# Performance work log

Measured on AMD Instinct MI355X. Metric: run time of the kernel, lower is better.

The kernel has to match this reference:

```python
import jax, jax.numpy as jnp
import numpy as np

B, S, D, H = 4, 2048, 512, 8


def _ln(x, g, b, eps=1e-5):
    m = x.mean(-1, keepdims=True)
    v = ((x - m) ** 2).mean(-1, keepdims=True)
    return (x - m) / jnp.sqrt(v + eps) * g + b


def setup_inputs() -> dict:
    key = jax.random.key(0)
    ks = iter(jax.random.split(key, 32))
    n = lambda shape, s=0.02: jax.random.normal(next(ks), shape, jnp.float32) * s
    z = lambda *shape: jnp.zeros(shape, jnp.float32)
    o = lambda *shape: jnp.ones(shape, jnp.float32)
    return {
        "x": jax.random.normal(next(ks), (B, S, D), jnp.float32),
        "x_prev": jax.random.normal(next(ks), (B, S, D), jnp.float32),
        "mu": jnp.float32(0.5),
        "in_proj_w": n((3 * D, D)), "in_proj_b": z(3 * D),
        "out_w": n((D, D)), "out_b": z(D),
        "ln1_g": o(D), "ln1_b": z(D),
        "time_mod": jnp.full((D,), 0.5, jnp.float32),
        "sm_ln_g": o(D), "sm_ln_b": z(D),
        "wr_w": n((D, D)), "wr_b": z(D),
        "wv_w": n((D, D)), "wv_b": z(D),
        "sc_ln_g": o(D), "sc_ln_b": z(D),
        "ln2_g": o(D), "ln2_b": z(D),
        "w1": n((4 * D, D)), "b1": z(4 * D),
        "w2": n((D, 4 * D)), "b2": z(D),
        "ln3_g": o(D), "ln3_b": z(D),
    }


def reference(x, x_prev, mu, in_proj_w, in_proj_b, out_w, out_b, ln1_g, ln1_b,
              time_mod, sm_ln_g, sm_ln_b, wr_w, wr_b, wv_w, wv_b,
              sc_ln_g, sc_ln_b, ln2_g, ln2_b, w1, b1, w2, b2, ln3_g, ln3_b):
    Bs, Sl, Dm = x.shape
    hd = Dm // H
    # Shift (x_prev is not None)
    shifted = mu * x + (1.0 - mu) * x_prev
    # Multihead self-attention (eval mode; dropout = identity)
    qkv = shifted @ in_proj_w.T + in_proj_b
    q, k, v = jnp.split(qkv, 3, axis=-1)
    q = q.reshape(Bs, Sl, H, hd)
    k = k.reshape(Bs, Sl, H, hd)
    v = v.reshape(Bs, Sl, H, hd)
    scores = jnp.einsum('bqhd,bkhd->bhqk', q, k) / jnp.sqrt(jnp.float32(hd))
    attn = jax.nn.softmax(scores, axis=-1)
    ao = jnp.einsum('bhqk,bkhd->bqhd', attn, v).reshape(Bs, Sl, Dm)
    ao = ao @ out_w.T + out_b
    x1 = _ln(shifted + ao, ln1_g, ln1_b)
    # SequenceMergingSeq with C = V = W = x1: sequential decayed running sums
    def step(carry, xt):  # xt: [B, D]
        a, b = carry
        decay = jax.nn.sigmoid(xt * time_mod)
        e = jnp.exp(xt)
        a = decay.mean(-1, keepdims=True) * a + e.sum(-1, keepdims=True)
        b = decay * b + e * xt
        return (a, b), b / (a + 1e-8)
    a0 = jnp.zeros((Bs, 1), x1.dtype)
    b0 = jnp.zeros((Bs, Dm), x1.dtype)
    _, outs = jax.lax.scan(step, (a0, b0), jnp.swapaxes(x1, 0, 1))  # [S,B,D]
    merged = _ln(jnp.swapaxes(outs, 0, 1), sm_ln_g, sm_ln_b)
    # StateCoupling
    coupled = _ln(jax.nn.sigmoid(merged @ wr_w.T + wr_b) * (merged @ wv_w.T + wv_b),
                  sc_ln_g, sc_ln_b)
    x2 = _ln(x1 + coupled, ln2_g, ln2_b)
    # FFN
    ffn = jax.nn.relu(x2 @ w1.T + b1) @ w2.T + b2
    return _ln(x2 + ffn, ln3_g, ln3_b)
```

## Files before the change

kernel.cpp:

```cpp
#include <hip/hip_runtime.h>
#include <math.h>

#define D_MODEL 512
#define SEQ     2048
#define BATCH   4
#define NH      8
#define HD      64
#define CHUNK   32
#define NCHUNK  64
#define M_TOK   (BATCH*SEQ)

typedef __attribute__((ext_vector_type(8))) short bhalf8;
typedef __attribute__((ext_vector_type(4))) float f32x4;

__device__ __forceinline__ float sigmoidf_(float x){ return 1.f/(1.f+expf(-x)); }

__device__ __forceinline__ unsigned short f2b(float f){
  unsigned u = __float_as_uint(f);
  u += 0x7FFFu + ((u>>16)&1u);
  return (unsigned short)(u>>16);
}
__device__ __forceinline__ float b2f(unsigned short h){
  return __uint_as_float(((unsigned)h)<<16);
}

__device__ __forceinline__ void gll16(const void* g, void* l){
  __builtin_amdgcn_global_load_lds(
      (const __attribute__((address_space(1))) unsigned int*)g,
      (__attribute__((address_space(3))) unsigned int*)l, 16, 0, 0);
}

__device__ __forceinline__ float exp2_hw(float x){
  float r;
  asm volatile("v_exp_f32 %0, %1" : "=v"(r) : "v"(x));
  return r;
}

__device__ __forceinline__ void block_sum2(float& a, float& b, float* lds){
  #pragma unroll
  for (int o=32;o>0;o>>=1){ a += __shfl_xor(a,o); b += __shfl_xor(b,o); }
  int w = threadIdx.x>>6, l = threadIdx.x&63;
  if (l==0){ lds[2*w]=a; lds[2*w+1]=b; }
  __syncthreads();
  float ta=0.f, tb=0.f; int nw = blockDim.x>>6;
  for (int i=0;i<nw;++i){ ta+=lds[2*i]; tb+=lds[2*i+1]; }
  a=ta; b=tb;
  __syncthreads();
}

__global__ void cvtshift_k(const float* __restrict__ s0,const float* __restrict__ s1,
                           const float* __restrict__ s2,const float* __restrict__ s3,
                           const float* __restrict__ s4,const float* __restrict__ s5,
                           unsigned short* __restrict__ d0,unsigned short* __restrict__ d1,
                           unsigned short* __restrict__ d2,unsigned short* __restrict__ d3,
                           unsigned short* __restrict__ d4,unsigned short* __restrict__ d5,
                           const float* __restrict__ x, const float* __restrict__ xp,
                           const float* __restrict__ mu, float* __restrict__ of,
                           unsigned short* __restrict__ ob){
  int t = blockIdx.x*blockDim.x + threadIdx.x;
  if (t < 917504){
    int j = t;
    const float* s; unsigned short* d;
    if (j < 196608){ s=s0; d=d0; }
    else if ((j-=196608) < 65536){ s=s1; d=d1; }
    else if ((j-=65536)  < 65536){ s=s2; d=d2; }
    else if ((j-=65536)  < 65536){ s=s3; d=d3; }
    else if ((j-=65536)  < 262144){ s=s4; d=d4; }
    else { j-=262144; s=s5; d=d5; }
    float4 v = ((const float4*)s)[j];
    unsigned a=f2b(v.x), b=f2b(v.y), c=f2b(v.z), e=f2b(v.w);
    uint2 p; p.x = a | (b<<16); p.y = c | (e<<16);
    ((uint2*)d)[j] = p;
  } else {
    int i = t - 917504;
    float m = mu[0];
    float4 a = ((const float4*)x)[i], p = ((const float4*)xp)[i];
    float4 r;
    r.x = m*a.x + (1.f-m)*p.x; r.y = m*a.y + (1.f-m)*p.y;
    r.z = m*a.z + (1.f-m)*p.z; r.w = m*a.w + (1.f-m)*p.w;
    ((float4*)of)[i] = r;
    unsigned A=f2b(r.x), B=f2b(r.y), C=f2b(r.z), E=f2b(r.w);
    uint2 q; q.x = A | (B<<16); q.y = C | (E<<16);
    ((uint2*)ob)[i] = q;
  }
}

template<int ACT, int OUTB>
__global__ __launch_bounds__(256) void mgemm_k(const unsigned short* __restrict__ A,
    const unsigned short* __restrict__ W, const float* __restrict__ bias,
    float* __restrict__ Yf, unsigned short* __restrict__ Yb, int Nd, int K){
  __shared__ unsigned short As[128*64];
  __shared__ unsigned short Bs[128*64];
  const int tid = threadIdx.x;
  const int w = tid>>6, lane = tid&63;
  const int l15 = lane&15, l4 = lane>>4;
  const int wr = w>>1, wc = w&1;
  const int nwg = gridDim.x*gridDim.y;
  const int orig = blockIdx.y*gridDim.x + blockIdx.x;
  const int swz = (orig&7)*(nwg>>3) + (orig>>3);
  const int bn = swz % gridDim.x;
  const int bm = swz / gridDim.x;

  const size_t Kb = (size_t)K*2;
  const int srow  = lane>>3;
  const int sbyte = ((lane&7)*16) ^ (srow<<4);
  const char* Ag = (const char*)A + (size_t)(bm*128)*Kb + sbyte;
  const char* Wg = (const char*)W + (size_t)(bn*128)*Kb + sbyte;

  f32x4 acc[4][4];
  const f32x4 z = {0.f,0.f,0.f,0.f};
  #pragma unroll
  for (int i=0;i<4;++i)
    #pragma unroll
    for (int j=0;j<4;++j) acc[i][j] = z;

  const int KT = K/64;
  for (int kt=0; kt<KT; ++kt){
    if (kt) __syncthreads();
    const size_t kOff = (size_t)kt*128;
    #pragma unroll
    for (int i=0;i<4;++i){
      int c = w*4 + i;
      int r = c*8 + srow;
      gll16(Ag + (size_t)r*Kb + kOff, (char*)As + c*1024);
      gll16(Wg + (size_t)r*Kb + kOff, (char*)Bs + c*1024);
    }
    __syncthreads();

    bhalf8 af[4][2], bf_[4][2];
    #pragma unroll
    for (int fr=0; fr<4; ++fr){
      int row = wr*64 + fr*16 + l15;
      #pragma unroll
      for (int ks=0; ks<2; ++ks){
        int byo = (l4*16 + ks*64) ^ ((row&7)<<4);
        af[fr][ks] = *(const bhalf8*)((const char*)As + row*128 + byo);
      }
    }
    #pragma unroll
    for (int fc=0; fc<4; ++fc){
      int row = wc*64 + fc*16 + l15;
      #pragma unroll
      for (int ks=0; ks<2; ++ks){
        int byo = (l4*16 + ks*64) ^ ((row&7)<<4);
        bf_[fc][ks] = *(const bhalf8*)((const char*)Bs + row*128 + byo);
      }
    }
    #pragma unroll
    for (int ks=0; ks<2; ++ks)
      #pragma unroll
      for (int fr=0; fr<4; ++fr)
        #pragma unroll
        for (int fc=0; fc<4; ++fc)
          acc[fr][fc] = __builtin_amdgcn_mfma_f32_16x16x32_bf16(af[fr][ks], bf_[fc][ks], acc[fr][fc], 0, 0, 0);
  }

  const int rowBase = bm*128 + wr*64;
  const int colBase = bn*128 + wc*64;
  #pragma unroll
  for (int fc=0; fc<4; ++fc){
    int col = colBase + fc*16 + l15;
    float bv = bias[col];
    #pragma unroll
    for (int fr=0; fr<4; ++fr){
      #pragma unroll
      for (int j=0; j<4; ++j){
        int row = rowBase + fr*16 + l4*4 + j;
        float v = acc[fr][fc][j] + bv;
        if (ACT) v = fmaxf(v, 0.f);
        if (OUTB) Yb[(size_t)row*Nd + col] = f2b(v);
        else      Yf[(size_t)row*Nd + col] = v;
      }
    }
  }
}

template<int ACT, int FUSE2, int OUTB>
__global__ __launch_bounds__(256) void mgemm64_k(const unsigned short* __restrict__ A,
    const unsigned short* __restrict__ W0, const unsigned short* __restrict__ W1v,
    const float* __restrict__ bias0, const float* __restrict__ bias1,
    float* __restrict__ Y0, float* __restrict__ Y1,
    unsigned short* __restrict__ Yb0, unsigned short* __restrict__ Yb1,
    int Nd, int K){
  __shared__ unsigned short As[128*64];
  __shared__ unsigned short Bs[64*64];
  const int tid = threadIdx.x;
  const int w = tid>>6, lane = tid&63;
  const int l15 = lane&15, l4 = lane>>4;
  const int wr = w>>1, wc = w&1;
  const int nwg = gridDim.x*gridDim.y;
  const int orig = blockIdx.y*gridDim.x + blockIdx.x;
  const int swz = (orig&7)*(nwg>>3) + (orig>>3);
  int bn = swz % gridDim.x;
  const int bm = swz / gridDim.x;
  const unsigned short* W = W0;
  const float* bias = bias0;
  float* Yf = Y0;
  unsigned short* Yb = Yb0;
  if (FUSE2 && bn >= 8){ W = W1v; bias = bias1; Yf = Y1; Yb = Yb1; bn -= 8; }

  const size_t Kb = (size_t)K*2;
  const int srow  = lane>>3;
  const int sbyte = ((lane&7)*16) ^ (srow<<4);
  const char* Ag = (const char*)A + (size_t)(bm*128)*Kb + sbyte;
  const char* Wg = (const char*)W + (size_t)(bn*64)*Kb + sbyte;

  f32x4 acc[4][2];
  const f32x4 z = {0.f,0.f,0.f,0.f};
  #pragma unroll
  for (int i=0;i<4;++i)
    #pragma unroll
    for (int j=0;j<2;++j) acc[i][j] = z;

  const int KT = K/64;
  for (int kt=0; kt<KT; ++kt){
    if (kt) __syncthreads();
    const size_t kOff = (size_t)kt*128;
    #pragma unroll
    for (int i=0;i<4;++i){
      int c = w*4 + i;
      int r = c*8 + srow;
      gll16(Ag + (size_t)r*Kb + kOff, (char*)As + c*1024);
    }
    #pragma unroll
    for (int i=0;i<2;++i){
      int c = w*2 + i;
      int r = c*8 + srow;
      gll16(Wg + (size_t)r*Kb + kOff, (char*)Bs + c*1024);
    }
    __syncthreads();

    bhalf8 af[4][2], bf_[2][2];
    #pragma unroll
    for (int fr=0; fr<4; ++fr){
      int row = wr*64 + fr*16 + l15;
      #pragma unroll
      for (int ks=0; ks<2; ++ks){
        int byo = (l4*16 + ks*64) ^ ((row&7)<<4);
        af[fr][ks] = *(const bhalf8*)((const char*)As + row*128 + byo);
      }
    }
    #pragma unroll
    for (int fc=0; fc<2; ++fc){
      int row = wc*32 + fc*16 + l15;
      #pragma unroll
      for (int ks=0; ks<2; ++ks){
        int byo = (l4*16 + ks*64) ^ ((row&7)<<4);
        bf_[fc][ks] = *(const bhalf8*)((const char*)Bs + row*128 + byo);
      }
    }
    #pragma unroll
    for (int ks=0; ks<2; ++ks)
      #pragma unroll
      for (int fr=0; fr<4; ++fr)
        #pragma unroll
        for (int fc=0; fc<2; ++fc)
          acc[fr][fc] = __builtin_amdgcn_mfma_f32_16x16x32_bf16(af[fr][ks], bf_[fc][ks], acc[fr][fc], 0, 0, 0);
  }

  const int rowBase = bm*128 + wr*64;
  const int colBase = bn*64 + wc*32;
  #pragma unroll
  for (int fc=0; fc<2; ++fc){
    int col = colBase + fc*16 + l15;
    float bv = bias[col];
    #pragma unroll
    for (int fr=0; fr<4; ++fr){
      #pragma unroll
      for (int j=0; j<4; ++j){
        int row = rowBase + fr*16 + l4*4 + j;
        float v = acc[fr][fc][j] + bv;
        if (ACT) v = fmaxf(v, 0.f);
        if (OUTB) Yb[(size_t)row*Nd + col] = f2b(v);
        else      Yf[(size_t)row*Nd + col] = v;
      }
    }
  }
}

__global__ __launch_bounds__(512, 4) void fattn_k(const unsigned short* __restrict__ qkv,
                                                  unsigned short* __restrict__ ao){
  __shared__ unsigned short Ks[2][64*64];
  __shared__ unsigned short Vt[2][64*64];
  __shared__ unsigned short Ps[128*64];
  const int nwg = gridDim.x*gridDim.y*gridDim.z;
  const int orig = (blockIdx.z*gridDim.y + blockIdx.y)*gridDim.x + blockIdx.x;
  const int swz = (orig&7)*(nwg>>3) + (orig>>3);
  const int qt = swz % gridDim.x;
  const int rem = swz / gridDim.x;
  const int h = rem % gridDim.y;
  const int b = rem / gridDim.y;
  const int tid = threadIdx.x, w = tid>>6, lane = tid&63;
  const int l15 = lane&15, l4 = lane>>4;
  const size_t rowB = 3072;
  const char* base = (const char*)qkv + (size_t)b*SEQ*rowB;
  const char* Kg = base + 1024 + h*128;
  const char* Vg = base + 2048 + h*128;
  const float C2 = 0.18033688f;

  bhalf8 qf[2];
  {
    const char* qrow = base + (size_t)(qt*128 + w*16 + l15)*rowB + h*128;
    qf[0] = *(const bhalf8*)(qrow + l4*16);
    qf[1] = *(const bhalf8*)(qrow + l4*16 + 64);
  }
  bhalf8 v1;
  {
    short o = (l15==0) ? (short)0x3F80 : (short)0;
    v1 = (bhalf8){o,o,o,o,o,o,o,o};
  }

  const f32x4 z = {0.f,0.f,0.f,0.f};
  f32x4 oa[4], ol = z;
  #pragma unroll
  for (int i=0;i<4;++i) oa[i] = z;
  float mj = -INFINITY;

  const int srow  = lane>>3;
  const int sbyte = ((lane&7)*16) ^ (srow<<4);
  const int vd = lane;
  const int vsel = (vd>>3)&1;

  unsigned short vload[8];
  {
    int r = w*8 + srow;
    gll16(Kg + (size_t)r*rowB + sbyte, (char*)Ks[0] + w*1024);
  }
  #pragma unroll
  for (int i=0;i<8;++i)
    vload[i] = *(const unsigned short*)(Vg + (size_t)(w*8 + i)*rowB + vd*2);

  int cur = 0;
  for (int kt=0; kt<SEQ/64; ++kt){
    #pragma unroll
    for (int i=0;i<2;++i){
      int p = i ^ vsel;
      unsigned lo = (unsigned)vload[p*4+0] | ((unsigned)vload[p*4+1]<<16);
      unsigned hi = (unsigned)vload[p*4+2] | ((unsigned)vload[p*4+3]<<16);
      uint2 pk; pk.x = lo; pk.y = hi;
      int byo = (w*16 + p*8) ^ ((vd&7)<<4);
      *(uint2*)((char*)Vt[cur] + vd*128 + byo) = pk;
    }
    __syncthreads();

    if (kt+1 < SEQ/64){
      int r = w*8 + srow;
      gll16(Kg + (size_t)((kt+1)*64 + r)*rowB + sbyte, (char*)Ks[cur^1] + w*1024);
      #pragma unroll
      for (int i=0;i<8;++i)
        vload[i] = *(const unsigned short*)(Vg + (size_t)((kt+1)*64 + w*8 + i)*rowB + vd*2);
    }

    bhalf8 kf[4][2];
    #pragma unroll
    for (int fc=0; fc<4; ++fc){
      int kr = fc*16 + l15;
      #pragma unroll
      for (int ks=0; ks<2; ++ks){
        int byo = (l4*16 + ks*64) ^ ((kr&7)<<4);
        kf[fc][ks] = *(const bhalf8*)((const char*)Ks[cur] + kr*128 + byo);
      }
    }
    f32x4 s[4];
    #pragma unroll
    for (int i=0;i<4;++i) s[i] = z;
    __builtin_amdgcn_s_setprio(1);
    #pragma unroll
    for (int ks=0; ks<2; ++ks)
      #pragma unroll
      for (int fc=0; fc<4; ++fc)
        s[fc] = __builtin_amdgcn_mfma_f32_16x16x32_bf16(kf[fc][ks], qf[ks], s[fc], 0, 0, 0);
    __builtin_amdgcn_s_setprio(0);

    {
      float rm0 = fmaxf(fmaxf(s[0][0],s[0][1]), fmaxf(s[0][2],s[0][3]));
      float rm1 = fmaxf(fmaxf(s[1][0],s[1][1]), fmaxf(s[1][2],s[1][3]));
      float rm2 = fmaxf(fmaxf(s[2][0],s[2][1]), fmaxf(s[2][2],s[2][3]));
      float rm3 = fmaxf(fmaxf(s[3][0],s[3][1]), fmaxf(s[3][2],s[3][3]));
      float rm = fmaxf(fmaxf(rm0,rm1), fmaxf(rm2,rm3));
      rm = fmaxf(rm, __shfl_xor(rm,16));
      rm = fmaxf(rm, __shfl_xor(rm,32));
      float tmax = rm * C2;
      if (__any(tmax > mj + 8.f)){
        float mn = fmaxf(mj, tmax);
        float sc = exp2_hw(mj - mn);
        mj = mn;
        float scj0 = __shfl(sc, l4*4+0), scj1 = __shfl(sc, l4*4+1);
        float scj2 = __shfl(sc, l4*4+2), scj3 = __shfl(sc, l4*4+3);
        #pragma unroll
        for (int fc=0; fc<4; ++fc){
          oa[fc][0] *= scj0; oa[fc][1] *= scj1;
          oa[fc][2] *= scj2; oa[fc][3] *= scj3;
        }
        ol[0] *= scj0; ol[1] *= scj1; ol[2] *= scj2; ol[3] *= scj3;
      }
      int qrow = w*16 + l15;
      #pragma unroll
      for (int fc=0; fc<4; ++fc){
        float p0 = exp2_hw(fmaf(C2, s[fc][0], -mj));
        float p1 = exp2_hw(fmaf(C2, s[fc][1], -mj));
        float p2 = exp2_hw(fmaf(C2, s[fc][2], -mj));
        float p3 = exp2_hw(fmaf(C2, s[fc][3], -mj));
        unsigned lo, hi;
        asm volatile("v_cvt_pk_bf16_f32 %0, %1, %2" : "=v"(lo) : "v"(p0), "v"(p1));
        asm volatile("v_cvt_pk_bf16_f32 %0, %1, %2" : "=v"(hi) : "v"(p2), "v"(p3));
        uint2 pk; pk.x = lo; pk.y = hi;
        int byo = (fc*32 + l4*8) ^ ((l15&7)<<4);
        *(uint2*)((char*)Ps + qrow*128 + byo) = pk;
      }
    }

    bhalf8 vf[4][2];
    #pragma unroll
    for (int fc=0; fc<4; ++fc){
      int d = fc*16 + l15;
      #pragma unroll
      for (int ks=0; ks<2; ++ks){
        int byo = (ks*64 + l4*16) ^ ((d&7)<<4);
        vf[fc][ks] = *(const bhalf8*)((const char*)Vt[cur] + d*128 + byo);
      }
    }
    {
      int qrow = w*16 + l15;
      bhalf8 pf[2];
      #pragma unroll
      for (int ks=0; ks<2; ++ks){
        int byo = (ks*64 + l4*16) ^ ((l15&7)<<4);
        pf[ks] = *(const bhalf8*)((const char*)Ps + qrow*128 + byo);
      }
      __builtin_amdgcn_s_setprio(1);
      #pragma unroll
      for (int ks=0; ks<2; ++ks){
        #pragma unroll
        for (int fc=0; fc<4; ++fc)
          oa[fc] = __builtin_amdgcn_mfma_f32_16x16x32_bf16(pf[ks], vf[fc][ks], oa[fc], 0, 0, 0);
        ol = __builtin_amdgcn_mfma_f32_16x16x32_bf16(pf[ks], v1, ol, 0, 0, 0);
      }
      __builtin_amdgcn_s_setprio(0);
    }
    cur ^= 1;
  }

  {
    float li[4];
    #pragma unroll
    for (int j=0;j<4;++j) li[j] = 1.f/__shfl(ol[j], l4<<4);
    #pragma unroll
    for (int fc=0; fc<4; ++fc){
      int col = h*64 + fc*16 + l15;
      size_t r0 = (size_t)(b*SEQ + qt*128 + w*16 + l4*4);
      ao[(r0+0)*D_MODEL + col] = f2b(oa[fc][0]*li[0]);
      ao[(r0+1)*D_MODEL + col] = f2b(oa[fc][1]*li[1]);
      ao[(r0+2)*D_MODEL + col] = f2b(oa[fc][2]*li[2]);
      ao[(r0+3)*D_MODEL + col] = f2b(oa[fc][3]*li[3]);
    }
  }
}

__global__ __launch_bounds__(256) void lnfin_k(const float* __restrict__ A,
    const unsigned short* __restrict__ Bp,
    const float* __restrict__ g, const float* __restrict__ be, float* __restrict__ outf){
  __shared__ float lds[16];
  const size_t off = (size_t)blockIdx.x * D_MODEL;
  const int tid = threadIdx.x;
  float a0 = A[off+tid]     + b2f(Bp[off+tid]);
  float a1 = A[off+tid+256] + b2f(Bp[off+tid+256]);
  float s1 = a0+a1, s2 = a0*a0+a1*a1;
  block_sum2(s1, s2, lds);
  float mean = s1 * (1.f/512.f);
  float var  = s2 * (1.f/512.f) - mean*mean;
  float rstd = rsqrtf(var + 1e-5f);
  outf[off+tid]     = (a0-mean)*rstd*g[tid]     + be[tid];
  outf[off+tid+256] = (a1-mean)*rstd*g[tid+256] + be[tid+256];
}

__global__ __launch_bounds__(256) void ln_scan_k(const float* __restrict__ A, const float* __restrict__ Bp,
    const float* __restrict__ g, const float* __restrict__ be, const float* __restrict__ tm,
    float* __restrict__ x1out, unsigned short* __restrict__ dec, unsigned short* __restrict__ u,
    float* __restrict__ dm, float* __restrict__ es){
  __shared__ float lds[16];
  const size_t row = blockIdx.x;
  const size_t off = row * D_MODEL;
  const int tid = threadIdx.x;
  float a0 = A[off+tid] + Bp[off+tid];
  float a1 = A[off+tid+256] + Bp[off+tid+256];
  float s1 = a0+a1, s2 = a0*a0+a1*a1;
  block_sum2(s1, s2, lds);
  float mean = s1 * (1.f/512.f);
  float var  = s2 * (1.f/512.f) - mean*mean;
  float rstd = rsqrtf(var + 1e-5f);
  float r0 = (a0-mean)*rstd*g[tid]     + be[tid];
  float r1 = (a1-mean)*rstd*g[tid+256] + be[tid+256];
  x1out[off+tid] = r0; x1out[off+tid+256] = r1;
  float dc0 = sigmoidf_(r0*tm[tid]), dc1 = sigmoidf_(r1*tm[tid+256]);
  float e0 = expf(r0), e1 = expf(r1);
  dec[off+tid]=f2b(dc0); dec[off+tid+256]=f2b(dc1);
  u[off+tid]=f2b(e0*r0); u[off+tid+256]=f2b(e1*r1);
  float dsum = dc0+dc1, esum = e0+e1;
  block_sum2(dsum, esum, lds);
  if (tid==0){ dm[row]=dsum*(1.f/512.f); es[row]=esum; }
}

__global__ __launch_bounds__(256) void ln2x_k(const unsigned short* __restrict__ R,
    const unsigned short* __restrict__ V, const float* __restrict__ X1,
    const float* __restrict__ g1, const float* __restrict__ b1_,
    const float* __restrict__ g2, const float* __restrict__ b2_,
    float* __restrict__ x2f, unsigned short* __restrict__ x2b){
  __shared__ float lds[16];
  const size_t off = (size_t)blockIdx.x * D_MODEL;
  const int tid = threadIdx.x;
  float a0 = sigmoidf_(b2f(R[off+tid]))*b2f(V[off+tid]);
  float a1 = sigmoidf_(b2f(R[off+tid+256]))*b2f(V[off+tid+256]);
  float s1 = a0+a1, s2 = a0*a0+a1*a1;
  block_sum2(s1, s2, lds);
  float mean = s1*(1.f/512.f);
  float var  = s2*(1.f/512.f) - mean*mean;
  float rstd = rsqrtf(var + 1e-5f);
  float c0 = (a0-mean)*rstd*g1[tid]     + b1_[tid];
  float c1 = (a1-mean)*rstd*g1[tid+256] + b1_[tid+256];
  float t0 = X1[off+tid] + c0, t1 = X1[off+tid+256] + c1;
  float u1 = t0+t1, u2 = t0*t0+t1*t1;
  block_sum2(u1, u2, lds);
  float mean2 = u1*(1.f/512.f);
  float var2  = u2*(1.f/512.f) - mean2*mean2;
  float rstd2 = rsqrtf(var2 + 1e-5f);
  float r0 = (t0-mean2)*rstd2*g2[tid]     + b2_[tid];
  float r1 = (t1-mean2)*rstd2*g2[tid+256] + b2_[tid+256];
  x2f[off+tid] = r0; x2f[off+tid+256] = r1;
  x2b[off+tid] = f2b(r0); x2b[off+tid+256] = f2b(r1);
}

__global__ __launch_bounds__(512) void bscan_p1(const unsigned short* __restrict__ decay,
    const unsigned short* __restrict__ u, float* __restrict__ Gc, float* __restrict__ Uc){
  const int c = blockIdx.x, b = blockIdx.y, d = threadIdx.x;
  size_t base = ((size_t)b*SEQ + (size_t)c*CHUNK)*D_MODEL + d;
  float G=1.f, U=0.f;
  for (int i=0;i<CHUNK;++i){
    float g  = b2f(decay[base + (size_t)i*D_MODEL]);
    float uu = b2f(u[base + (size_t)i*D_MODEL]);
    U = g*U + uu; G = g*G;
  }
  size_t idx = ((size_t)b*NCHUNK + c)*D_MODEL + d;
  Gc[idx]=G; Uc[idx]=U;
}

__global__ __launch_bounds__(512) void scan2_k(const float* __restrict__ Gc, const float* __restrict__ Uc,
    float* __restrict__ binit, const float* __restrict__ dm, const float* __restrict__ es,
    float* __restrict__ a_out){
  __shared__ float sG[512], sU[512];
  if (blockIdx.x < 4){
    const int b = blockIdx.x, d = threadIdx.x;
    float cur = 0.f;
    for (int c=0;c<NCHUNK;++c){
      size_t idx = ((size_t)b*NCHUNK + c)*D_MODEL + d;
      binit[idx] = cur;
      cur = Gc[idx]*cur + Uc[idx];
    }
  } else {
    const int b = blockIdx.x - 4, tid = threadIdx.x;
    const float* dmb = dm + (size_t)b*SEQ;
    const float* esb = es + (size_t)b*SEQ;
    const int t0 = tid*4;
    float gi[4], ui[4];
    #pragma unroll
    for (int i=0;i<4;++i){ gi[i]=dmb[t0+i]; ui[i]=esb[t0+i]; }
    float G=1.f, U=0.f;
    #pragma unroll
    for (int i=0;i<4;++i){ U = gi[i]*U + ui[i]; G *= gi[i]; }
    sG[tid]=G; sU[tid]=U;
    __syncthreads();
    for (int off=1; off<512; off<<=1){
      float pg=1.f, pu=0.f;
      bool act = tid >= off;
      if (act){ pg = sG[tid-off]; pu = sU[tid-off]; }
      __syncthreads();
      if (act){ sU[tid] = sG[tid]*pu + sU[tid]; sG[tid] = sG[tid]*pg; }
      __syncthreads();
    }
    float a = (tid==0) ? 0.f : sU[tid-1];
    #pragma unroll
    for (int i=0;i<4;++i){ a = gi[i]*a + ui[i]; a_out[(size_t)b*SEQ + t0 + i] = a; }
  }
}

__global__ __launch_bounds__(512) void p3ln_k(const unsigned short* __restrict__ decay,
    const unsigned short* __restrict__ u,
    const float* __restrict__ binit, const float* __restrict__ a,
    const float* __restrict__ g, const float* __restrict__ be,
    unsigned short* __restrict__ mb){
  __shared__ float lds[16];
  const int c = blockIdx.x, b = blockIdx.y, d = threadIdx.x;
  size_t base = ((size_t)b*SEQ + (size_t)c*CHUNK)*D_MODEL + d;
  float bv = binit[((size_t)b*NCHUNK + c)*D_MODEL + d];
  float gg = g[d], bb = be[d];
  for (int i=0;i<CHUNK;++i){
    float gd = b2f(decay[base + (size_t)i*D_MODEL]);
    float uu = b2f(u[base + (size_t)i*D_MODEL]);
    bv = gd*bv + uu;
    float av = a[(size_t)b*SEQ + (size_t)c*CHUNK + i];
    float val = bv / (av + 1e-8f);
    float s1 = val, s2 = val*val;
    block_sum2(s1, s2, lds);
    float mean = s1*(1.f/512.f);
    float var  = s2*(1.f/512.f) - mean*mean;
    float rstd = rsqrtf(var + 1e-5f);
    mb[base + (size_t)i*D_MODEL] = f2b((val-mean)*rstd*gg + bb);
  }
}

extern "C" void kernel_launch(void* const* d_in, const int* in_sizes, int n_in,
                              void* d_out, int out_size, void* d_ws, size_t ws_size,
                              hipStream_t stream){
  const float* x     = (const float*)d_in[0];
  const float* xp    = (const float*)d_in[1];
  const float* mu    = (const float*)d_in[2];
  const float* in_w  = (const float*)d_in[3];
  const float* in_b  = (const float*)d_in[4];
  const float* out_w = (const float*)d_in[5];
  const float* out_b = (const float*)d_in[6];
  const float* ln1_g = (const float*)d_in[7];
  const float* ln1_b = (const float*)d_in[8];
  const float* tm    = (const float*)d_in[9];
  const float* sm_g  = (const float*)d_in[10];
  const float* sm_b  = (const float*)d_in[11];
  const float* wr_w  = (const float*)d_in[12];
  const float* wr_b  = (const float*)d_in[13];
  const float* wv_w  = (const float*)d_in[14];
  const float* wv_b  = (const float*)d_in[15];
  const float* sc_g  = (const float*)d_in[16];
  const float* sc_b  = (const float*)d_in[17];
  const float* ln2_g = (const float*)d_in[18];
  const float* ln2_b = (const float*)d_in[19];
  const float* w1    = (const float*)d_in[20];
  const float* b1    = (const float*)d_in[21];
  const float* w2    = (const float*)d_in[22];
  const float* b2    = (const float*)d_in[23];
  const float* ln3_g = (const float*)d_in[24];
  const float* ln3_b = (const float*)d_in[25];
  float* out = (float*)d_out;
  float* ws  = (float*)d_ws;

  const size_t N = (size_t)M_TOK*D_MODEL;
  float* S0f = ws;
  float* S1f = ws + N;
  float* S2f = ws + 2*N;
  float* EX  = ws + 3*N;
  float* dm    = EX;
  float* es    = EX + 8192;
  float* aarr  = EX + 16384;
  float* Gc    = EX + 24576;
  float* Uc    = Gc + 131072;
  float* binit = Uc + 131072;

  unsigned short* SB = (unsigned short*)(ws + 3*N + N/4);
  unsigned short* Wq = SB;
  unsigned short* Wo = Wq + 786432;
  unsigned short* Wr = Wo + 262144;
  unsigned short* Wv = Wr + 262144;
  unsigned short* W1 = Wv + 262144;
  unsigned short* W2 = W1 + 1048576;
  unsigned short* Xb = W2 + 1048576;
  unsigned short* Mb = Xb + N;
  unsigned short* U  = Mb + N;
  unsigned short* Qb  = U;
  unsigned short* AOb = U + 12*1024*1024;
  unsigned short* ub   = U;
  unsigned short* decb = U + 12*1024*1024;
  unsigned short* Rb   = U;
  unsigned short* Vb   = U + 4*1024*1024;
  unsigned short* Hb   = U;
  unsigned short* Fb   = Mb;

  cvtshift_k<<<7680, 256, 0, stream>>>(in_w, out_w, wr_w, wv_w, w1, w2,
                                       Wq, Wo, Wr, Wv, W1, W2,
                                       x, xp, mu, S0f, Xb);
  mgemm_k<0,1><<<dim3(12,64), 256, 0, stream>>>(Xb, Wq, in_b, nullptr, Qb, 1536, 512);
  fattn_k<<<dim3(SEQ/128, NH, BATCH), 512, 0, stream>>>(Qb, AOb);
  mgemm64_k<0,0,0><<<dim3(8,64), 256, 0, stream>>>(AOb, Wo, nullptr, out_b, nullptr,
                                                   S1f, nullptr, nullptr, nullptr, 512, 512);
  ln_scan_k<<<M_TOK, 256, 0, stream>>>(S0f, S1f, ln1_g, ln1_b, tm, S2f, decb, ub, dm, es);
  bscan_p1<<<dim3(NCHUNK, BATCH), 512, 0, stream>>>(decb, ub, Gc, Uc);
  scan2_k<<<8, 512, 0, stream>>>(Gc, Uc, binit, dm, es, aarr);
  p3ln_k<<<dim3(NCHUNK, BATCH), 512, 0, stream>>>(decb, ub, binit, aarr, sm_g, sm_b, Mb);
  mgemm64_k<0,1,1><<<dim3(16,64), 256, 0, stream>>>(Mb, Wr, Wv, wr_b, wv_b,
                                                    nullptr, nullptr, Rb, Vb, 512, 512);
  ln2x_k<<<M_TOK, 256, 0, stream>>>(Rb, Vb, S2f, sc_g, sc_b, ln2_g, ln2_b, S0f, Xb);
  mgemm_k<1,1><<<dim3(16,64), 256, 0, stream>>>(Xb, W1, b1, nullptr, Hb, 2048, 512);
  mgemm64_k<0,0,1><<<dim3(8,64), 256, 0, stream>>>(Hb, W2, nullptr, b2, nullptr,
                                                   nullptr, nullptr, Fb, nullptr, 512, 2048);
  lnfin_k<<<M_TOK, 256, 0, stream>>>(S0f, Fb, ln3_g, ln3_b, out);
}
```

Measured before the change: 262.0 us.

## Store residual streams in bf16, pack elementwise kernels, split-K the FFN down GEMM

```diff
diff --git a/kernel.cpp b/kernel.cpp
--- a/kernel.cpp
+++ b/kernel.cpp
@@ -22,6 +22,11 @@
 }
 __device__ __forceinline__ float b2f(unsigned short h){
   return __uint_as_float(((unsigned)h)<<16);
+}
+__device__ __forceinline__ float blo(unsigned v){ return __uint_as_float(v<<16); }
+__device__ __forceinline__ float bhi(unsigned v){ return __uint_as_float(v & 0xFFFF0000u); }
+__device__ __forceinline__ unsigned bpack(float a, float b){
+  return (unsigned)f2b(a) | ((unsigned)f2b(b)<<16);
 }
 
 __device__ __forceinline__ void gll16(const void* g, void* l){
@@ -55,7 +60,7 @@
                            unsigned short* __restrict__ d2,unsigned short* __restrict__ d3,
                            unsigned short* __restrict__ d4,unsigned short* __restrict__ d5,
                            const float* __restrict__ x, const float* __restrict__ xp,
-                           const float* __restrict__ mu, float* __restrict__ of,
+                           const float* __restrict__ mu,
                            unsigned short* __restrict__ ob){
   int t = blockIdx.x*blockDim.x + threadIdx.x;
   if (t < 917504){
@@ -68,8 +73,7 @@
     else if ((j-=65536)  < 262144){ s=s4; d=d4; }
     else { j-=262144; s=s5; d=d5; }
     float4 v = ((const float4*)s)[j];
-    unsigned a=f2b(v.x), b=f2b(v.y), c=f2b(v.z), e=f2b(v.w);
-    uint2 p; p.x = a | (b<<16); p.y = c | (e<<16);
+    uint2 p; p.x = bpack(v.x, v.y); p.y = bpack(v.z, v.w);
     ((uint2*)d)[j] = p;
   } else {
     int i = t - 917504;
@@ -78,9 +82,7 @@
     float4 r;
     r.x = m*a.x + (1.f-m)*p.x; r.y = m*a.y + (1.f-m)*p.y;
     r.z = m*a.z + (1.f-m)*p.z; r.w = m*a.w + (1.f-m)*p.w;
-    ((float4*)of)[i] = r;
-    unsigned A=f2b(r.x), B=f2b(r.y), C=f2b(r.z), E=f2b(r.w);
-    uint2 q; q.x = A | (B<<16); q.y = C | (E<<16);
+    uint2 q; q.x = bpack(r.x, r.y); q.y = bpack(r.z, r.w);
     ((uint2*)ob)[i] = q;
   }
 }
@@ -175,11 +177,10 @@
   }
 }
 
-template<int ACT, int FUSE2, int OUTB>
+template<int ACT, int FUSE2, int SPLITK>
 __global__ __launch_bounds__(256) void mgemm64_k(const unsigned short* __restrict__ A,
     const unsigned short* __restrict__ W0, const unsigned short* __restrict__ W1v,
     const float* __restrict__ bias0, const float* __restrict__ bias1,
-    float* __restrict__ Y0, float* __restrict__ Y1,
     unsigned short* __restrict__ Yb0, unsigned short* __restrict__ Yb1,
     int Nd, int K){
   __shared__ unsigned short As[128*64];
@@ -195,15 +196,18 @@
   const int bm = swz / gridDim.x;
   const unsigned short* W = W0;
   const float* bias = bias0;
-  float* Yf = Y0;
   unsigned short* Yb = Yb0;
-  if (FUSE2 && bn >= 8){ W = W1v; bias = bias1; Yf = Y1; Yb = Yb1; bn -= 8; }
-
+  int half = 0;
+  if (FUSE2 && bn >= 8){ W = W1v; bias = bias1; Yb = Yb1; bn -= 8; }
+  if (SPLITK && bn >= 8){ half = 1; Yb = Yb1; bn -= 8; }
+
+  const int Ksr = SPLITK ? (K>>1) : K;
   const size_t Kb = (size_t)K*2;
+  const size_t hOff = (size_t)half * Ksr * 2;
   const int srow  = lane>>3;
   const int sbyte = ((lane&7)*16) ^ (srow<<4);
-  const char* Ag = (const char*)A + (size_t)(bm*128)*Kb + sbyte;
-  const char* Wg = (const char*)W + (size_t)(bn*64)*Kb + sbyte;
+  const char* Ag = (const char*)A + (size_t)(bm*128)*Kb + hOff + sbyte;
+  const char* Wg = (const char*)W + (size_t)(bn*64)*Kb + hOff + sbyte;
 
   f32x4 acc[4][2];
   const f32x4 z = {0.f,0.f,0.f,0.f};
@@ -212,7 +216,7 @@
     #pragma unroll
     for (int j=0;j<2;++j) acc[i][j] = z;
 
-  const int KT = K/64;
+  const int KT = Ksr/64;
   for (int kt=0; kt<KT; ++kt){
     if (kt) __syncthreads();
     const size_t kOff = (size_t)kt*128;
@@ -263,7 +267,7 @@
   #pragma unroll
   for (int fc=0; fc<2; ++fc){
     int col = colBase + fc*16 + l15;
-    float bv = bias[col];
+    float bv = (SPLITK && half) ? 0.f : bias[col];
     #pragma unroll
     for (int fr=0; fr<4; ++fr){
       #pragma unroll
@@ -271,8 +275,7 @@
         int row = rowBase + fr*16 + l4*4 + j;
         float v = acc[fr][fc][j] + bv;
         if (ACT) v = fmaxf(v, 0.f);
-        if (OUTB) Yb[(size_t)row*Nd + col] = f2b(v);
-        else      Yf[(size_t)row*Nd + col] = v;
+        Yb[(size_t)row*Nd + col] = f2b(v);
       }
     }
   }
@@ -457,91 +460,106 @@
   }
 }
 
-__global__ __launch_bounds__(256) void lnfin_k(const float* __restrict__ A,
-    const unsigned short* __restrict__ Bp,
+__global__ __launch_bounds__(256) void lnfin_k(const unsigned int* __restrict__ X2b,
+    const unsigned int* __restrict__ F0, const unsigned int* __restrict__ F1,
     const float* __restrict__ g, const float* __restrict__ be, float* __restrict__ outf){
   __shared__ float lds[16];
-  const size_t off = (size_t)blockIdx.x * D_MODEL;
+  const size_t off2 = (size_t)blockIdx.x * 256;
   const int tid = threadIdx.x;
-  float a0 = A[off+tid]     + b2f(Bp[off+tid]);
-  float a1 = A[off+tid+256] + b2f(Bp[off+tid+256]);
+  unsigned xv = X2b[off2+tid], f0 = F0[off2+tid], f1 = F1[off2+tid];
+  float a0 = blo(xv) + blo(f0) + blo(f1);
+  float a1 = bhi(xv) + bhi(f0) + bhi(f1);
   float s1 = a0+a1, s2 = a0*a0+a1*a1;
   block_sum2(s1, s2, lds);
   float mean = s1 * (1.f/512.f);
   float var  = s2 * (1.f/512.f) - mean*mean;
   float rstd = rsqrtf(var + 1e-5f);
-  outf[off+tid]     = (a0-mean)*rstd*g[tid]     + be[tid];
-  outf[off+tid+256] = (a1-mean)*rstd*g[tid+256] + be[tid+256];
-}
-
-__global__ __launch_bounds__(256) void ln_scan_k(const float* __restrict__ A, const float* __restrict__ Bp,
+  float2 gg = ((const float2*)g)[tid], bb = ((const float2*)be)[tid];
+  float2 r;
+  r.x = (a0-mean)*rstd*gg.x + bb.x;
+  r.y = (a1-mean)*rstd*gg.y + bb.y;
+  ((float2*)outf)[off2+tid] = r;
+}
+
+__global__ __launch_bounds__(256) void ln_scan_k(const unsigned int* __restrict__ Ab,
+    const unsigned int* __restrict__ Pb,
     const float* __restrict__ g, const float* __restrict__ be, const float* __restrict__ tm,
-    float* __restrict__ x1out, unsigned short* __restrict__ dec, unsigned short* __restrict__ u,
+    unsigned int* __restrict__ x1b, unsigned int* __restrict__ dec, unsigned int* __restrict__ u,
     float* __restrict__ dm, float* __restrict__ es){
   __shared__ float lds[16];
   const size_t row = blockIdx.x;
-  const size_t off = row * D_MODEL;
+  const size_t off2 = row * 256;
   const int tid = threadIdx.x;
-  float a0 = A[off+tid] + Bp[off+tid];
-  float a1 = A[off+tid+256] + Bp[off+tid+256];
+  unsigned av = Ab[off2+tid], pv = Pb[off2+tid];
+  float a0 = blo(av) + blo(pv);
+  float a1 = bhi(av) + bhi(pv);
   float s1 = a0+a1, s2 = a0*a0+a1*a1;
   block_sum2(s1, s2, lds);
   float mean = s1 * (1.f/512.f);
   float var  = s2 * (1.f/512.f) - mean*mean;
   float rstd = rsqrtf(var + 1e-5f);
-  float r0 = (a0-mean)*rstd*g[tid]     + be[tid];
-  float r1 = (a1-mean)*rstd*g[tid+256] + be[tid+256];
-  x1out[off+tid] = r0; x1out[off+tid+256] = r1;
-  float dc0 = sigmoidf_(r0*tm[tid]), dc1 = sigmoidf_(r1*tm[tid+256]);
+  float2 gg = ((const float2*)g)[tid], bb = ((const float2*)be)[tid], tt = ((const float2*)tm)[tid];
+  float r0 = (a0-mean)*rstd*gg.x + bb.x;
+  float r1 = (a1-mean)*rstd*gg.y + bb.y;
+  x1b[off2+tid] = bpack(r0, r1);
+  float dc0 = sigmoidf_(r0*tt.x), dc1 = sigmoidf_(r1*tt.y);
   float e0 = expf(r0), e1 = expf(r1);
-  dec[off+tid]=f2b(dc0); dec[off+tid+256]=f2b(dc1);
-  u[off+tid]=f2b(e0*r0); u[off+tid+256]=f2b(e1*r1);
+  dec[off2+tid] = bpack(dc0, dc1);
+  u[off2+tid]   = bpack(e0*r0, e1*r1);
   float dsum = dc0+dc1, esum = e0+e1;
   block_sum2(dsum, esum, lds);
   if (tid==0){ dm[row]=dsum*(1.f/512.f); es[row]=esum; }
 }
 
-__global__ __launch_bounds__(256) void ln2x_k(const unsigned short* __restrict__ R,
-    const unsigned short* __restrict__ V, const float* __restrict__ X1,
+__global__ __launch_bounds__(256) void ln2x_k(const unsigned int* __restrict__ R,
+    const unsigned int* __restrict__ V, const unsigned int* __restrict__ X1,
     const float* __restrict__ g1, const float* __restrict__ b1_,
     const float* __restrict__ g2, const float* __restrict__ b2_,
-    float* __restrict__ x2f, unsigned short* __restrict__ x2b){
+    unsigned int* __restrict__ x2b){
   __shared__ float lds[16];
-  const size_t off = (size_t)blockIdx.x * D_MODEL;
+  const size_t off2 = (size_t)blockIdx.x * 256;
   const int tid = threadIdx.x;
-  float a0 = sigmoidf_(b2f(R[off+tid]))*b2f(V[off+tid]);
-  float a1 = sigmoidf_(b2f(R[off+tid+256]))*b2f(V[off+tid+256]);
+  unsigned rv = R[off2+tid], vv = V[off2+tid];
+  float a0 = sigmoidf_(blo(rv))*blo(vv);
+  float a1 = sigmoidf_(bhi(rv))*bhi(vv);
   float s1 = a0+a1, s2 = a0*a0+a1*a1;
   block_sum2(s1, s2, lds);
   float mean = s1*(1.f/512.f);
   float var  = s2*(1.f/512.f) - mean*mean;
   float rstd = rsqrtf(var + 1e-5f);
-  float c0 = (a0-mean)*rstd*g1[tid]     + b1_[tid];
-  float c1 = (a1-mean)*rstd*g1[tid+256] + b1_[tid+256];
-  float t0 = X1[off+tid] + c0, t1 = X1[off+tid+256] + c1;
+  float2 g1v = ((const float2*)g1)[tid], b1v = ((const float2*)b1_)[tid];
+  float c0 = (a0-mean)*rstd*g1v.x + b1v.x;
+  float c1 = (a1-mean)*rstd*g1v.y + b1v.y;
+  unsigned x1v = X1[off2+tid];
+  float t0 = blo(x1v) + c0, t1 = bhi(x1v) + c1;
   float u1 = t0+t1, u2 = t0*t0+t1*t1;
   block_sum2(u1, u2, lds);
   float mean2 = u1*(1.f/512.f);
   float var2  = u2*(1.f/512.f) - mean2*mean2;
   float rstd2 = rsqrtf(var2 + 1e-5f);
-  float r0 = (t0-mean2)*rstd2*g2[tid]     + b2_[tid];
-  float r1 = (t1-mean2)*rstd2*g2[tid+256] + b2_[tid+256];
-  x2f[off+tid] = r0; x2f[off+tid+256] = r1;
-  x2b[off+tid] = f2b(r0); x2b[off+tid+256] = f2b(r1);
-}
-
-__global__ __launch_bounds__(512) void bscan_p1(const unsigned short* __restrict__ decay,
-    const unsigned short* __restrict__ u, float* __restrict__ Gc, float* __restrict__ Uc){
-  const int c = blockIdx.x, b = blockIdx.y, d = threadIdx.x;
-  size_t base = ((size_t)b*SEQ + (size_t)c*CHUNK)*D_MODEL + d;
-  float G=1.f, U=0.f;
+  float2 g2v = ((const float2*)g2)[tid], b2v = ((const float2*)b2_)[tid];
+  float r0 = (t0-mean2)*rstd2*g2v.x + b2v.x;
+  float r1 = (t1-mean2)*rstd2*g2v.y + b2v.y;
+  x2b[off2+tid] = bpack(r0, r1);
+}
+
+__global__ __launch_bounds__(256) void bscan_p1(const unsigned int* __restrict__ decay,
+    const unsigned int* __restrict__ u, float* __restrict__ Gc, float* __restrict__ Uc){
+  const int c = blockIdx.x, b = blockIdx.y, t = threadIdx.x;
+  size_t base2 = ((size_t)b*SEQ + (size_t)c*CHUNK)*256 + t;
+  float G0=1.f, G1=1.f, U0=0.f, U1=0.f;
   for (int i=0;i<CHUNK;++i){
-    float g  = b2f(decay[base + (size_t)i*D_MODEL]);
-    float uu = b2f(u[base + (size_t)i*D_MODEL]);
-    U = g*U + uu; G = g*G;
-  }
-  size_t idx = ((size_t)b*NCHUNK + c)*D_MODEL + d;
-  Gc[idx]=G; Uc[idx]=U;
+    unsigned dv = decay[base2 + (size_t)i*256];
+    unsigned uv = u[base2 + (size_t)i*256];
+    float g0 = blo(dv), g1 = bhi(dv);
+    U0 = g0*U0 + blo(uv); G0 *= g0;
+    U1 = g1*U1 + bhi(uv); G1 *= g1;
+  }
+  size_t idx2 = ((size_t)b*NCHUNK + c)*256 + t;
+  float2 gv; gv.x=G0; gv.y=G1;
+  float2 uv2; uv2.x=U0; uv2.y=U1;
+  ((float2*)Gc)[idx2] = gv;
+  ((float2*)Uc)[idx2] = uv2;
 }
 
 __global__ __launch_bounds__(512) void scan2_k(const float* __restrict__ Gc, const float* __restrict__ Uc,
@@ -583,28 +601,31 @@
   }
 }
 
-__global__ __launch_bounds__(512) void p3ln_k(const unsigned short* __restrict__ decay,
-    const unsigned short* __restrict__ u,
+__global__ __launch_bounds__(256) void p3ln_k(const unsigned int* __restrict__ decay,
+    const unsigned int* __restrict__ u,
     const float* __restrict__ binit, const float* __restrict__ a,
     const float* __restrict__ g, const float* __restrict__ be,
-    unsigned short* __restrict__ mb){
+    unsigned int* __restrict__ mb){
   __shared__ float lds[16];
-  const int c = blockIdx.x, b = blockIdx.y, d = threadIdx.x;
-  size_t base = ((size_t)b*SEQ + (size_t)c*CHUNK)*D_MODEL + d;
-  float bv = binit[((size_t)b*NCHUNK + c)*D_MODEL + d];
-  float gg = g[d], bb = be[d];
+  const int c = blockIdx.x, b = blockIdx.y, t = threadIdx.x;
+  size_t base2 = ((size_t)b*SEQ + (size_t)c*CHUNK)*256 + t;
+  float2 bv = ((const float2*)binit)[((size_t)b*NCHUNK + c)*256 + t];
+  float2 gg = ((const float2*)g)[t], bb = ((const float2*)be)[t];
   for (int i=0;i<CHUNK;++i){
-    float gd = b2f(decay[base + (size_t)i*D_MODEL]);
-    float uu = b2f(u[base + (size_t)i*D_MODEL]);
-    bv = gd*bv + uu;
+    unsigned dv = decay[base2 + (size_t)i*256];
+    unsigned uv = u[base2 + (size_t)i*256];
+    bv.x = blo(dv)*bv.x + blo(uv);
+    bv.y = bhi(dv)*bv.y + bhi(uv);
     float av = a[(size_t)b*SEQ + (size_t)c*CHUNK + i];
-    float val = bv / (av + 1e-8f);
-    float s1 = val, s2 = val*val;
+    float inv = 1.f/(av + 1e-8f);
+    float v0 = bv.x*inv, v1 = bv.y*inv;
+    float s1 = v0+v1, s2 = v0*v0+v1*v1;
     block_sum2(s1, s2, lds);
     float mean = s1*(1.f/512.f);
     float var  = s2*(1.f/512.f) - mean*mean;
     float rstd = rsqrtf(var + 1e-5f);
-    mb[base + (size_t)i*D_MODEL] = f2b((val-mean)*rstd*gg + bb);
+    mb[base2 + (size_t)i*256] = bpack((v0-mean)*rstd*gg.x + bb.x,
+                                      (v1-mean)*rstd*gg.y + bb.y);
   }
 }
 
@@ -641,9 +662,10 @@
   float* ws  = (float*)d_ws;
 
   const size_t N = (size_t)M_TOK*D_MODEL;
-  float* S0f = ws;
-  float* S1f = ws + N;
-  float* S2f = ws + 2*N;
+  unsigned short* Pb  = (unsigned short*)ws;
+  unsigned short* X1b = (unsigned short*)ws + N;
+  unsigned short* F0  = (unsigned short*)(ws + N);
+  unsigned short* F1  = (unsigned short*)(ws + N) + N;
   float* EX  = ws + 3*N;
   float* dm    = EX;
   float* es    = EX + 8192;
@@ -669,24 +691,30 @@
   unsigned short* Rb   = U;
   unsigned short* Vb   = U + 4*1024*1024;
   unsigned short* Hb   = U;
-  unsigned short* Fb   = Mb;
 
   cvtshift_k<<<7680, 256, 0, stream>>>(in_w, out_w, wr_w, wv_w, w1, w2,
                                        Wq, Wo, Wr, Wv, W1, W2,
-                                       x, xp, mu, S0f, Xb);
+                                       x, xp, mu, Xb);
   mgemm_k<0,1><<<dim3(12,64), 256, 0, stream>>>(Xb, Wq, in_b, nullptr, Qb, 1536, 512);
   fattn_k<<<dim3(SEQ/128, NH, BATCH), 512, 0, stream>>>(Qb, AOb);
   mgemm64_k<0,0,0><<<dim3(8,64), 256, 0, stream>>>(AOb, Wo, nullptr, out_b, nullptr,
-                                                   S1f, nullptr, nullptr, nullptr, 512, 512);
-  ln_scan_k<<<M_TOK, 256, 0, stream>>>(S0f, S1f, ln1_g, ln1_b, tm, S2f, decb, ub, dm, es);
-  bscan_p1<<<dim3(NCHUNK, BATCH), 512, 0, stream>>>(decb, ub, Gc, Uc);
+                                                   Pb, nullptr, 512, 512);
+  ln_scan_k<<<M_TOK, 256, 0, stream>>>((const unsigned int*)Xb, (const unsigned int*)Pb,
+                                       ln1_g, ln1_b, tm,
+                                       (unsigned int*)X1b, (unsigned int*)decb, (unsigned int*)ub,
+                                       dm, es);
+  bscan_p1<<<dim3(NCHUNK, BATCH), 256, 0, stream>>>((const unsigned int*)decb, (const unsigned int*)ub, Gc, Uc);
   scan2_k<<<8, 512, 0, stream>>>(Gc, Uc, binit, dm, es, aarr);
-  p3ln_k<<<dim3(NCHUNK, BATCH), 512, 0, stream>>>(decb, ub, binit, aarr, sm_g, sm_b, Mb);
-  mgemm64_k<0,1,1><<<dim3(16,64), 256, 0, stream>>>(Mb, Wr, Wv, wr_b, wv_b,
-                                                    nullptr, nullptr, Rb, Vb, 512, 512);
-  ln2x_k<<<M_TOK, 256, 0, stream>>>(Rb, Vb, S2f, sc_g, sc_b, ln2_g, ln2_b, S0f, Xb);
+  p3ln_k<<<dim3(NCHUNK, BATCH), 256, 0, stream>>>((const unsigned int*)decb, (const unsigned int*)ub,
+                                                  binit, aarr, sm_g, sm_b, (unsigned int*)Mb);
+  mgemm64_k<0,1,0><<<dim3(16,64), 256, 0, stream>>>(Mb, Wr, Wv, wr_b, wv_b,
+                                                    Rb, Vb, 512, 512);
+  ln2x_k<<<M_TOK, 256, 0, stream>>>((const unsigned int*)Rb, (const unsigned int*)Vb,
+                                    (const unsigned int*)X1b,
+                                    sc_g, sc_b, ln2_g, ln2_b, (unsigned int*)Xb);
   mgemm_k<1,1><<<dim3(16,64), 256, 0, stream>>>(Xb, W1, b1, nullptr, Hb, 2048, 512);
-  mgemm64_k<0,0,1><<<dim3(8,64), 256, 0, stream>>>(Hb, W2, nullptr, b2, nullptr,
-                                                   nullptr, nullptr, Fb, nullptr, 512, 2048);
-  lnfin_k<<<M_TOK, 256, 0, stream>>>(S0f, Fb, ln3_g, ln3_b, out);
-}
+  mgemm64_k<0,0,1><<<dim3(16,64), 256, 0, stream>>>(Hb, W2, nullptr, b2, nullptr,
+                                                    F0, F1, 512, 2048);
+  lnfin_k<<<M_TOK, 256, 0, stream>>>((const unsigned int*)Xb, (const unsigned int*)F0,
+                                     (const unsigned int*)F1, ln3_g, ln3_b, out);
+}
```

After: 252.3 us. 3.7% less time.
